# Performance work log

Hardware: AMD Instinct MI355X
Metric: run time of the kernel (lower is better)

The kernel has to match this reference:

```python
import jax, jax.numpy as jnp
import numpy as np

B, L, E, H = 4, 2048, 512, 8


def setup_inputs() -> dict:
    key = jax.random.key(0)
    ks = jax.random.split(key, 12)
    s = 0.02
    inp = {
        "values": jax.random.normal(ks[0], (B, L, E), jnp.float32),
        "keys": jax.random.normal(ks[1], (B, L, E), jnp.float32),
        "queries": jax.random.normal(ks[2], (B, L, E), jnp.float32),
    }
    mask = jax.random.randint(ks[3], (B, L, H, H), 0, 2, jnp.int32)
    # guarantee at least one unmasked entry per softmax row to avoid NaN rows
    mask = mask.at[..., 0].set(1)
    inp["mask"] = mask
    # Linear(E, E*H) weights stored as (in, out); torch uses y = x @ W.T + b
    inp["Wv"] = jax.random.normal(ks[4], (E, E * H), jnp.float32) * s
    inp["bv"] = jnp.zeros((E * H,), jnp.float32)
    inp["Wk"] = jax.random.normal(ks[5], (E, E * H), jnp.float32) * s
    inp["bk"] = jnp.zeros((E * H,), jnp.float32)
    inp["Wq"] = jax.random.normal(ks[6], (E, E * H), jnp.float32) * s
    inp["bq"] = jnp.zeros((E * H,), jnp.float32)
    inp["Wo"] = jax.random.normal(ks[7], (E * H, E), jnp.float32) * s
    inp["bo"] = jnp.zeros((E,), jnp.float32)
    return inp


def reference(values, keys, queries, mask, Wv, bv, Wk, bk, Wq, bq, Wo, bo):
    b, l, e = queries.shape
    h = Wq.shape[1] // e

    def proj(x, W, bias):
        # (B,L,E) -> (B,L,H,E) -> transpose(1,2) -> (B,H,L,E)
        return (x @ W + bias).reshape(b, -1, h, e).transpose(0, 2, 1, 3)

    v = proj(values, Wv, bv)
    k = proj(keys, Wk, bk)
    q = proj(queries, Wq, bq)
    # Faithful to source: einsum labels applied to the TRANSPOSED (B,H,L,E)
    # tensors, so 'q'/'k' bind to the heads axis and 'h' binds to seq axis.
    # energy: (B, L, H, H) -- head-vs-head scores at each position.
    energy = jnp.einsum('nqhd,nkhd->nhqk', q, k)
    energy = jnp.where(mask == 0, -jnp.inf, energy)
    attn = jax.nn.softmax(energy / jnp.sqrt(jnp.float32(e)), axis=3)
    # out of einsum: (B, H, L, E); raw row-major reshape to (B, L, H*E)
    out = jnp.einsum('nhql,nlhd->nqhd', attn, v).reshape(b, -1, h * e)
    return out @ Wo + bo
```

## Files before the change

### kernel.cpp

```cpp
#include <hip/hip_runtime.h>
#include <stdint.h>

typedef __attribute__((ext_vector_type(4))) float f32x4;
typedef __attribute__((ext_vector_type(8))) __bf16 bf16x8;

__device__ __forceinline__ unsigned short f2bf(float f) {
  union { float f; uint32_t u; } v; v.f = f;
  uint32_t u = v.u;
  return (unsigned short)((u + 0x7FFFu + ((u >> 16) & 1u)) >> 16);
}
__device__ __forceinline__ float bflo(uint32_t u) {
  union { uint32_t u; float f; } v; v.u = u << 16; return v.f;
}
__device__ __forceinline__ float bfhi(uint32_t u) {
  union { uint32_t u; float f; } v; v.u = u & 0xffff0000u; return v.f;
}

__device__ __forceinline__ void async_copy16(void* lds, const void* g) {
  __builtin_amdgcn_global_load_lds(
      (const __attribute__((address_space(1))) void*)g,
      (__attribute__((address_space(3))) void*)lds,
      16, 0, 0);
}

__global__ void cvt3_f32_bf16(const float* __restrict__ in0,
                              const float* __restrict__ in1,
                              const float* __restrict__ in2,
                              uint32_t* __restrict__ out, int n) {
  const float* in = (blockIdx.y == 0) ? in0 : (blockIdx.y == 1) ? in1 : in2;
  uint32_t* o = out + (size_t)blockIdx.y * (n / 2);
  int i = blockIdx.x * blockDim.x + threadIdx.x;
  int idx = i * 8;
  if (idx >= n) return;
  float4 a = *(const float4*)(in + idx);
  float4 b = *(const float4*)(in + idx + 4);
  uint4 ov;
  ov.x = f2bf(a.x) | ((uint32_t)f2bf(a.y) << 16);
  ov.y = f2bf(a.z) | ((uint32_t)f2bf(a.w) << 16);
  ov.z = f2bf(b.x) | ((uint32_t)f2bf(b.y) << 16);
  ov.w = f2bf(b.z) | ((uint32_t)f2bf(b.w) << 16);
  *(uint4*)(o + i * 4) = ov;
}

__global__ void transpose3_to_bf16(const float* __restrict__ in0,
                                   const float* __restrict__ in1,
                                   const float* __restrict__ in2,
                                   unsigned short* __restrict__ out,
                                   int R, int C) {
  const float* in = (blockIdx.z == 0) ? in0 : (blockIdx.z == 1) ? in1 : in2;
  unsigned short* o = out + (size_t)blockIdx.z * ((size_t)R * C);
  __shared__ float tile[32][33];
  int c0 = blockIdx.x * 32, r0 = blockIdx.y * 32;
  int tx = threadIdx.x, ty = threadIdx.y;
  #pragma unroll
  for (int rr = 0; rr < 32; rr += 8)
    tile[ty + rr][tx] = in[(size_t)(r0 + ty + rr) * C + c0 + tx];
  __syncthreads();
  #pragma unroll
  for (int rr = 0; rr < 32; rr += 8)
    o[(size_t)(c0 + ty + rr) * R + r0 + tx] = f2bf(tile[tx][ty + rr]);
}

__global__ void transpose_to_bf16(const float* __restrict__ in,
                                  unsigned short* __restrict__ out,
                                  int R, int C) {
  __shared__ float tile[32][33];
  int c0 = blockIdx.x * 32, r0 = blockIdx.y * 32;
  int tx = threadIdx.x, ty = threadIdx.y;
  #pragma unroll
  for (int rr = 0; rr < 32; rr += 8)
    tile[ty + rr][tx] = in[(size_t)(r0 + ty + rr) * C + c0 + tx];
  __syncthreads();
  #pragma unroll
  for (int rr = 0; rr < 32; rr += 8)
    out[(size_t)(c0 + ty + rr) * R + r0 + tx] = f2bf(tile[tx][ty + rr]);
}

template <int NK, int NN, bool PARTIAL>
__global__ __launch_bounds__(512, 2) void gemm256(
    const unsigned short* __restrict__ A,
    const unsigned short* __restrict__ Bt,
    const float* __restrict__ bias,
    void* __restrict__ Cout,
    int Mt, int NtG, int KC, int Kfull) {
  constexpr int TT = NK * NN;
  static_assert(TT >= 3, "schedule needs >=3 tiles");
  __shared__ unsigned short lds[2 * 2 * 256 * 64];

  const int nwg = Mt * NtG * KC;
  const int cpx = nwg >> 3;
  const int bid = blockIdx.x;
  const int nb = (bid & 7) * cpx + (bid >> 3);
  const int kc = nb / (Mt * NtG);
  const int r2 = nb % (Mt * NtG);
  const int bm = r2 / NtG;
  const int ng = r2 % NtG;
  const int N = NtG * NN * 256;
  const size_t koff = (size_t)kc * (NK * 64);

  const int tid = threadIdx.x;
  const int wv = tid >> 6, ln = tid & 63;
  const int wm = wv >> 2, wn = wv & 3;

  f32x4 acc[8][4] = {};
  bf16x8 af[4][2];
  bf16x8 bfb[2][2];

  auto stage_A = [&](int h, int tau) {
    const int kt = tau % NK;
    #pragma unroll
    for (int r = 0; r < 2; ++r) {
      const int rb = r * 128 + h * 64 + wv * 8;
      const int row = rb + (ln >> 3);
      const int kcs = (ln & 7) ^ (row & 7);
      const unsigned short* g =
          A + (size_t)(bm * 256 + row) * Kfull + koff + kt * 64 + kcs * 8;
      char* dst = (char*)lds + (size_t)(tau & 1) * 65536 + rb * 128;
      async_copy16(dst, g);
    }
  };
  auto stage_B = [&](int h, int tau) {
    const int kt = tau % NK;
    const int bnn = ng * NN + tau / NK;
    #pragma unroll
    for (int r = 0; r < 2; ++r) {
      const int s = r * 2 + (wv >> 2);
      const int rb = s * 64 + h * 32 + (wv & 3) * 8;
      const int row = rb + (ln >> 3);
      const int kcs = (ln & 7) ^ (row & 7);
      const unsigned short* g =
          Bt + (size_t)(bnn * 256 + row) * Kfull + koff + kt * 64 + kcs * 8;
      char* dst = (char*)lds + (size_t)(tau & 1) * 65536 + 32768 + rb * 128;
      async_copy16(dst, g);
    }
  };
  auto load_af = [&](int mh, const char* buf) {
    #pragma unroll
    for (int f = 0; f < 4; ++f) {
      const int lr = wm * 128 + (mh * 4 + f) * 16 + (ln & 15);
      #pragma unroll
      for (int s = 0; s < 2; ++s) {
        const int kq = s * 4 + (ln >> 4);
        af[f][s] = *(const bf16x8*)(buf + lr * 128 + ((kq ^ (lr & 7)) * 16));
      }
    }
  };
  auto load_bf = [&](int nh, const char* buf) {
    #pragma unroll
    for (int gq = 0; gq < 2; ++gq) {
      const int lr = wn * 64 + (nh * 2 + gq) * 16 + (ln & 15);
      #pragma unroll
      for (int s = 0; s < 2; ++s) {
        const int kq = s * 4 + (ln >> 4);
        bfb[gq][s] =
            *(const bf16x8*)(buf + 32768 + lr * 128 + ((kq ^ (lr & 7)) * 16));
      }
    }
  };
  auto mfma_quad = [&](int mh, int nh) {
    __builtin_amdgcn_sched_barrier(0);
    __builtin_amdgcn_s_barrier();
    __builtin_amdgcn_sched_barrier(0);
    __builtin_amdgcn_s_setprio(1);
    #pragma unroll
    for (int f = 0; f < 4; ++f)
      #pragma unroll
      for (int gq = 0; gq < 2; ++gq)
        #pragma unroll
        for (int s = 0; s < 2; ++s)
          acc[mh * 4 + f][nh * 2 + gq] = __builtin_amdgcn_mfma_f32_16x16x32_bf16(
              bfb[gq][s], af[f][s], acc[mh * 4 + f][nh * 2 + gq], 0, 0, 0);
    __builtin_amdgcn_s_setprio(0);
    __builtin_amdgcn_sched_barrier(0);
  };
  auto epilogue = [&](int nt) {
    const int m0 = bm * 256 + wm * 128 + (ln & 15);
    const int n0 = (ng * NN + nt) * 256 + wn * 64 + ((ln >> 4) << 2);
    if (PARTIAL) {
      float* Cp = (float*)Cout + (size_t)kc * ((size_t)Mt * 256) * N;
      #pragma unroll
      for (int f = 0; f < 8; ++f) {
        const int row = m0 + f * 16;
        #pragma unroll
        for (int g = 0; g < 4; ++g)
          *(f32x4*)(Cp + (size_t)row * N + n0 + g * 16) = acc[f][g];
      }
    } else {
      unsigned short* C = (unsigned short*)Cout;
      #pragma unroll
      for (int f = 0; f < 8; ++f) {
        const int row = m0 + f * 16;
        #pragma unroll
        for (int g = 0; g < 4; ++g) {
          const int col = n0 + g * 16;
          float4 bv = *(const float4*)(bias + col);
          uint2 o;
          o.x = f2bf(acc[f][g][0] + bv.x) | ((uint32_t)f2bf(acc[f][g][1] + bv.y) << 16);
          o.y = f2bf(acc[f][g][2] + bv.z) | ((uint32_t)f2bf(acc[f][g][3] + bv.w) << 16);
          *(uint2*)(C + (size_t)row * N + col) = o;
        }
      }
    }
    #pragma unroll
    for (int f = 0; f < 8; ++f)
      #pragma unroll
      for (int g = 0; g < 4; ++g)
        acc[f][g] = (f32x4){0.f, 0.f, 0.f, 0.f};
  };

  stage_A(0, 0); stage_B(1, 0); stage_A(1, 0); stage_B(0, 0);
  stage_A(0, 1); stage_B(1, 1); stage_A(1, 1);
  asm volatile("s_waitcnt vmcnt(6)" ::: "memory");
  __builtin_amdgcn_sched_barrier(0);
  __builtin_amdgcn_s_barrier();

  for (int tau = 0; tau < TT; ++tau) {
    const char* buf = (const char*)lds + (size_t)(tau & 1) * 65536;
    load_af(0, buf); load_bf(0, buf);
    if (tau + 1 < TT) stage_B(0, tau + 1);
    mfma_quad(0, 0);
    __builtin_amdgcn_s_barrier();
    load_bf(1, buf);
    if (tau + 2 < TT) stage_A(0, tau + 2);
    mfma_quad(0, 1);
    __builtin_amdgcn_s_barrier();
    load_af(1, buf);
    if (tau + 2 < TT) stage_B(1, tau + 2);
    mfma_quad(1, 1);
    __builtin_amdgcn_s_barrier();
    load_bf(0, buf);
    if (tau + 2 < TT) stage_A(1, tau + 2);
    mfma_quad(1, 0);
    if (tau + 2 < TT) {
      asm volatile("s_waitcnt vmcnt(6)" ::: "memory");
    } else if (tau + 1 < TT) {
      asm volatile("s_waitcnt vmcnt(0)" ::: "memory");
    }
    __builtin_amdgcn_sched_barrier(0);
    __builtin_amdgcn_s_barrier();
    if ((tau + 1) % NK == 0) epilogue(tau / NK);
  }
}

__global__ void reduce4_bias(const float* __restrict__ p,
                             const float* __restrict__ bo,
                             float* __restrict__ out) {
  const size_t S = (size_t)8192 * 512;
  size_t i = ((size_t)blockIdx.x * 256 + threadIdx.x) * 4;
  float4 a = *(const float4*)(p + i);
  float4 b = *(const float4*)(p + S + i);
  float4 c = *(const float4*)(p + 2 * S + i);
  float4 d = *(const float4*)(p + 3 * S + i);
  float4 bb = *(const float4*)(bo + (int)(i & 511));
  float4 o;
  o.x = a.x + b.x + c.x + d.x + bb.x;
  o.y = a.y + b.y + c.y + d.y + bb.y;
  o.z = a.z + b.z + c.z + d.z + bb.z;
  o.w = a.w + b.w + c.w + d.w + bb.w;
  *(float4*)(out + i) = o;
}

__global__ __launch_bounds__(256) void energy_mfma(
    const unsigned short* __restrict__ Q,
    const unsigned short* __restrict__ Kb,
    const int* __restrict__ mask,
    float* __restrict__ P) {
  const int wave = threadIdx.x >> 6, ln = threadIdx.x & 63;
  const int t2 = (blockIdx.x * 4 + wave) * 2;
  const int r16 = ln & 15;
  const int g = ln >> 4;
  const size_t rowoff = (size_t)(t2 + (r16 >> 3)) * 4096 + (r16 & 7) * 512 + g * 8;
  const unsigned short* qb = Q + rowoff;
  const unsigned short* kb = Kb + rowoff;

  f32x4 acc = {};
  #pragma unroll
  for (int s = 0; s < 16; ++s) {
    bf16x8 qf = *(const bf16x8*)(qb + s * 32);
    bf16x8 kf = *(const bf16x8*)(kb + s * 32);
    acc = __builtin_amdgcn_mfma_f32_16x16x32_bf16(qf, kf, acc, 0, 0, 0);
  }

  const int ct = r16 >> 3, j = r16 & 7;
  const bool valid = ((g >> 1) == ct);
  const int tok = t2 + ct;
  float pv[4];
  #pragma unroll
  for (int r = 0; r < 4; ++r) {
    const int i = (g & 1) * 4 + r;
    float e = acc[r] * 0.044194173824159216f;
    int mk = 1;
    if (valid) mk = mask[(size_t)tok * 64 + i * 8 + j];
    if (mk == 0) e = -1e30f;
    float m = e;
    m = fmaxf(m, __shfl_xor(m, 1, 64));
    m = fmaxf(m, __shfl_xor(m, 2, 64));
    m = fmaxf(m, __shfl_xor(m, 4, 64));
    float p = __expf(e - m);
    float sum = p;
    sum += __shfl_xor(sum, 1, 64);
    sum += __shfl_xor(sum, 2, 64);
    sum += __shfl_xor(sum, 4, 64);
    pv[r] = p / sum;
  }
  if (valid) {
    #pragma unroll
    for (int r = 0; r < 4; ++r) {
      const int i = (g & 1) * 4 + r;
      P[(size_t)tok * 64 + i * 8 + j] = pv[r];
    }
  }
}

__global__ __launch_bounds__(256) void pv_kernel(
    const float* __restrict__ P,
    const unsigned short* __restrict__ Vb,
    unsigned short* __restrict__ out2) {
  const int wave = threadIdx.x >> 6, lane = threadIdx.x & 63;
  const int t = blockIdx.x * 4 + wave;
  const unsigned short* Vr = Vb + (size_t)t * 4096;
  float att = P[(size_t)t * 64 + lane];

  uint4 v4[8];
  #pragma unroll
  for (int jj = 0; jj < 8; ++jj)
    v4[jj] = *(const uint4*)(Vr + jj * 512 + lane * 8);

  const int nb = t >> 11, l = t & 2047;
  const size_t tok_base = (size_t)nb * 8388608 + (size_t)(l >> 3) * 4096 +
                          (size_t)(l & 7) * 512 + lane * 8;
  #pragma unroll
  for (int hh = 0; hh < 8; ++hh) {
    float accv[8] = {0.f, 0.f, 0.f, 0.f, 0.f, 0.f, 0.f, 0.f};
    #pragma unroll
    for (int jj = 0; jj < 8; ++jj) {
      float a = __shfl(att, hh * 8 + jj, 64);
      accv[0] += a * bflo(v4[jj].x); accv[1] += a * bfhi(v4[jj].x);
      accv[2] += a * bflo(v4[jj].y); accv[3] += a * bfhi(v4[jj].y);
      accv[4] += a * bflo(v4[jj].z); accv[5] += a * bfhi(v4[jj].z);
      accv[6] += a * bflo(v4[jj].w); accv[7] += a * bfhi(v4[jj].w);
    }
    uint4 o;
    o.x = f2bf(accv[0]) | ((uint32_t)f2bf(accv[1]) << 16);
    o.y = f2bf(accv[2]) | ((uint32_t)f2bf(accv[3]) << 16);
    o.z = f2bf(accv[4]) | ((uint32_t)f2bf(accv[5]) << 16);
    o.w = f2bf(accv[6]) | ((uint32_t)f2bf(accv[7]) << 16);
    *(uint4*)(out2 + tok_base + (size_t)hh * 1048576) = o;
  }
}

extern "C" void kernel_launch(void* const* d_in, const int* in_sizes, int n_in,
                              void* d_out, int out_size, void* d_ws, size_t ws_size,
                              hipStream_t stream) {
  const float* values  = (const float*)d_in[0];
  const float* keys    = (const float*)d_in[1];
  const float* queries = (const float*)d_in[2];
  const int*   mask    = (const int*)d_in[3];
  const float* Wv = (const float*)d_in[4];
  const float* bv = (const float*)d_in[5];
  const float* Wk = (const float*)d_in[6];
  const float* bk = (const float*)d_in[7];
  const float* Wq = (const float*)d_in[8];
  const float* bq = (const float*)d_in[9];
  const float* Wo = (const float*)d_in[10];
  const float* bo = (const float*)d_in[11];

  unsigned short* xv  = (unsigned short*)d_ws;
  unsigned short* xk  = xv + 8192 * 512;
  unsigned short* xq  = xk + 8192 * 512;
  unsigned short* Wvt = xq + 8192 * 512;
  unsigned short* Wkt = Wvt + 4096 * 512;
  unsigned short* Wqt = Wkt + 4096 * 512;
  unsigned short* Wot = Wqt + 4096 * 512;
  float*          P   = (float*)(Wot + 4096 * 512);
  unsigned short* bufA = (unsigned short*)(P + 8192 * 64);
  unsigned short* bufB = bufA + (size_t)8192 * 4096;

  const int nx = 8192 * 512;
  cvt3_f32_bf16<<<dim3(nx / 8 / 256, 3), 256, 0, stream>>>(
      values, keys, queries, (uint32_t*)xv, nx);

  transpose3_to_bf16<<<dim3(4096 / 32, 512 / 32, 3), dim3(32, 8), 0, stream>>>(
      Wv, Wk, Wq, Wvt, 512, 4096);
  transpose_to_bf16<<<dim3(512 / 32, 4096 / 32), dim3(32, 8), 0, stream>>>(
      Wo, Wot, 4096, 512);

  gemm256<8, 2, false><<<256, 512, 0, stream>>>(xq, Wqt, bq, bufA, 32, 8, 1, 512);
  gemm256<8, 2, false><<<256, 512, 0, stream>>>(xk, Wkt, bk, bufB, 32, 8, 1, 512);

  energy_mfma<<<8192 / 8, 256, 0, stream>>>(bufA, bufB, mask, P);

  gemm256<8, 2, false><<<256, 512, 0, stream>>>(xv, Wvt, bv, bufA, 32, 8, 1, 512);

  pv_kernel<<<8192 / 4, 256, 0, stream>>>(P, bufA, bufB);

  gemm256<16, 1, true><<<256, 512, 0, stream>>>(bufB, Wot, nullptr, (float*)bufA,
                                                32, 2, 4, 4096);
  reduce4_bias<<<4096, 256, 0, stream>>>((float*)bufA, bo, (float*)d_out);
}
```

Before: 271.6 us.

## Fuse Q and K projection GEMMs into one launch and add smaller-tile V GEMM

Merges the Q and K projection GEMMs into a single dual-matrix launch of 512 workgroups, each picking its source matrices from its N-group index. This doubles the number of workgroups in flight, since 256 workgroups at 2 per CU underfill the GPU. The V projection moves to a new 128x128-tile GEMM kernel with 2048 workgroups and simple double buffering, trading per-tile reuse for more parallelism. The new kernel waits on vmcnt(0) every tile, so global-load latency may be less hidden than in the deeper-pipelined 256 kernel.

```diff
diff --git a/kernel.cpp b/kernel.cpp
--- a/kernel.cpp
+++ b/kernel.cpp
@@ -76,15 +76,19 @@
     out[(size_t)(c0 + ty + rr) * R + r0 + tx] = f2bf(tile[tx][ty + rr]);
 }
 
-template <int NK, int NN, bool PARTIAL>
+template <int NK, int NN, bool PARTIAL, bool DUAL>
 __global__ __launch_bounds__(512, 2) void gemm256(
     const unsigned short* __restrict__ A,
     const unsigned short* __restrict__ Bt,
     const float* __restrict__ bias,
     void* __restrict__ Cout,
+    const unsigned short* __restrict__ A2,
+    const unsigned short* __restrict__ Bt2,
+    const float* __restrict__ bias2,
+    void* __restrict__ Cout2,
     int Mt, int NtG, int KC, int Kfull) {
   constexpr int TT = NK * NN;
-  static_assert(TT >= 3, "schedule needs >=3 tiles");
+  static_assert(TT >= 4, "schedule needs >=4 tiles");
   __shared__ unsigned short lds[2 * 2 * 256 * 64];
 
   const int nwg = Mt * NtG * KC;
@@ -95,8 +99,15 @@
   const int r2 = nb % (Mt * NtG);
   const int bm = r2 / NtG;
   const int ng = r2 % NtG;
-  const int N = NtG * NN * 256;
+  const int mat = DUAL ? (ng >> 3) : 0;
+  const int ngm = DUAL ? (ng & 7) : ng;
+  const int N = (DUAL ? (NtG >> 1) : NtG) * NN * 256;
   const size_t koff = (size_t)kc * (NK * 64);
+
+  const unsigned short* Asrc = (DUAL && mat) ? A2 : A;
+  const unsigned short* Bsrc = (DUAL && mat) ? Bt2 : Bt;
+  const float* biasd = (DUAL && mat) ? bias2 : bias;
+  void* Cd = (DUAL && mat) ? Cout2 : Cout;
 
   const int tid = threadIdx.x;
   const int wv = tid >> 6, ln = tid & 63;
@@ -114,14 +125,14 @@
       const int row = rb + (ln >> 3);
       const int kcs = (ln & 7) ^ (row & 7);
       const unsigned short* g =
-          A + (size_t)(bm * 256 + row) * Kfull + koff + kt * 64 + kcs * 8;
+          Asrc + (size_t)(bm * 256 + row) * Kfull + koff + kt * 64 + kcs * 8;
       char* dst = (char*)lds + (size_t)(tau & 1) * 65536 + rb * 128;
       async_copy16(dst, g);
     }
   };
   auto stage_B = [&](int h, int tau) {
     const int kt = tau % NK;
-    const int bnn = ng * NN + tau / NK;
+    const int bnn = ngm * NN + tau / NK;
     #pragma unroll
     for (int r = 0; r < 2; ++r) {
       const int s = r * 2 + (wv >> 2);
@@ -129,7 +140,7 @@
       const int row = rb + (ln >> 3);
       const int kcs = (ln & 7) ^ (row & 7);
       const unsigned short* g =
-          Bt + (size_t)(bnn * 256 + row) * Kfull + koff + kt * 64 + kcs * 8;
+          Bsrc + (size_t)(bnn * 256 + row) * Kfull + koff + kt * 64 + kcs * 8;
       char* dst = (char*)lds + (size_t)(tau & 1) * 65536 + 32768 + rb * 128;
       async_copy16(dst, g);
     }
@@ -175,9 +186,9 @@
   };
   auto epilogue = [&](int nt) {
     const int m0 = bm * 256 + wm * 128 + (ln & 15);
-    const int n0 = (ng * NN + nt) * 256 + wn * 64 + ((ln >> 4) << 2);
+    const int n0 = (ngm * NN + nt) * 256 + wn * 64 + ((ln >> 4) << 2);
     if (PARTIAL) {
-      float* Cp = (float*)Cout + (size_t)kc * ((size_t)Mt * 256) * N;
+      float* Cp = (float*)Cd + (size_t)kc * ((size_t)Mt * 256) * N;
       #pragma unroll
       for (int f = 0; f < 8; ++f) {
         const int row = m0 + f * 16;
@@ -186,14 +197,14 @@
           *(f32x4*)(Cp + (size_t)row * N + n0 + g * 16) = acc[f][g];
       }
     } else {
-      unsigned short* C = (unsigned short*)Cout;
+      unsigned short* C = (unsigned short*)Cd;
       #pragma unroll
       for (int f = 0; f < 8; ++f) {
         const int row = m0 + f * 16;
         #pragma unroll
         for (int g = 0; g < 4; ++g) {
           const int col = n0 + g * 16;
-          float4 bv = *(const float4*)(bias + col);
+          float4 bv = *(const float4*)(biasd + col);
           uint2 o;
           o.x = f2bf(acc[f][g][0] + bv.x) | ((uint32_t)f2bf(acc[f][g][1] + bv.y) << 16);
           o.y = f2bf(acc[f][g][2] + bv.z) | ((uint32_t)f2bf(acc[f][g][3] + bv.w) << 16);
@@ -242,6 +253,106 @@
   }
 }
 
+template <int NK>
+__global__ __launch_bounds__(256, 2) void gemm128(
+    const unsigned short* __restrict__ A,
+    const unsigned short* __restrict__ Bt,
+    const float* __restrict__ bias,
+    unsigned short* __restrict__ Cout,
+    int Mt, int Nt, int Kfull) {
+  static_assert((NK % 2) == 0, "even NK");
+  __shared__ unsigned short lds[2 * 2 * 128 * 64];
+  const int nwg = Mt * Nt;
+  const int cpx = nwg >> 3;
+  const int bid = blockIdx.x;
+  const int nb = (bid & 7) * cpx + (bid >> 3);
+  const int bm = nb / Nt, bn = nb % Nt;
+  const int N = Nt * 128;
+  const int tid = threadIdx.x;
+  const int wv = tid >> 6, ln = tid & 63;
+  const int wm = wv >> 1, wn = wv & 1;
+
+  f32x4 acc[4][4] = {};
+  bf16x8 af[4][2], bfb[4][2];
+  char* const lds0 = (char*)lds;
+  char* const lds1 = (char*)lds + 32768;
+
+  auto stage = [&](int t, char* dst) {
+    #pragma unroll
+    for (int r = 0; r < 4; ++r) {
+      const int c = wv * 4 + r;
+      const int row = c * 8 + (ln >> 3);
+      const int kcs = (ln & 7) ^ (row & 7);
+      const unsigned short* ga =
+          A + (size_t)(bm * 128 + row) * Kfull + t * 64 + kcs * 8;
+      async_copy16(dst + c * 1024, ga);
+      const unsigned short* gb =
+          Bt + (size_t)(bn * 128 + row) * Kfull + t * 64 + kcs * 8;
+      async_copy16(dst + 16384 + c * 1024, gb);
+    }
+  };
+  auto tile_body = [&](int t, const char* buf, char* obuf) {
+    if (t + 1 < NK) stage(t + 1, obuf);
+    #pragma unroll
+    for (int f = 0; f < 4; ++f) {
+      const int lr = wm * 64 + f * 16 + (ln & 15);
+      #pragma unroll
+      for (int s = 0; s < 2; ++s) {
+        const int kq = s * 4 + (ln >> 4);
+        af[f][s] = *(const bf16x8*)(buf + lr * 128 + ((kq ^ (lr & 7)) * 16));
+      }
+    }
+    #pragma unroll
+    for (int c = 0; c < 4; ++c) {
+      const int lr = wn * 64 + c * 16 + (ln & 15);
+      #pragma unroll
+      for (int s = 0; s < 2; ++s) {
+        const int kq = s * 4 + (ln >> 4);
+        bfb[c][s] = *(const bf16x8*)(buf + 16384 + lr * 128 + ((kq ^ (lr & 7)) * 16));
+      }
+    }
+    __builtin_amdgcn_s_setprio(1);
+    #pragma unroll
+    for (int f = 0; f < 4; ++f)
+      #pragma unroll
+      for (int c = 0; c < 4; ++c)
+        #pragma unroll
+        for (int s = 0; s < 2; ++s)
+          acc[f][c] = __builtin_amdgcn_mfma_f32_16x16x32_bf16(
+              bfb[c][s], af[f][s], acc[f][c], 0, 0, 0);
+    __builtin_amdgcn_s_setprio(0);
+    asm volatile("s_waitcnt vmcnt(0)" ::: "memory");
+    __builtin_amdgcn_sched_barrier(0);
+    __builtin_amdgcn_s_barrier();
+  };
+
+  stage(0, lds0);
+  asm volatile("s_waitcnt vmcnt(0)" ::: "memory");
+  __builtin_amdgcn_sched_barrier(0);
+  __builtin_amdgcn_s_barrier();
+
+  for (int it = 0; it < NK / 2; ++it) {
+    tile_body(2 * it,     lds0, lds1);
+    tile_body(2 * it + 1, lds1, lds0);
+  }
+
+  const int m0 = bm * 128 + wm * 64 + (ln & 15);
+  const int n0 = bn * 128 + wn * 64 + ((ln >> 4) << 2);
+  #pragma unroll
+  for (int f = 0; f < 4; ++f) {
+    const int row = m0 + f * 16;
+    #pragma unroll
+    for (int c = 0; c < 4; ++c) {
+      const int col = n0 + c * 16;
+      float4 bv = *(const float4*)(bias + col);
+      uint2 o;
+      o.x = f2bf(acc[f][c][0] + bv.x) | ((uint32_t)f2bf(acc[f][c][1] + bv.y) << 16);
+      o.y = f2bf(acc[f][c][2] + bv.z) | ((uint32_t)f2bf(acc[f][c][3] + bv.w) << 16);
+      *(uint2*)(Cout + (size_t)row * N + col) = o;
+    }
+  }
+}
+
 __global__ void reduce4_bias(const float* __restrict__ p,
                              const float* __restrict__ bo,
                              float* __restrict__ out) {
@@ -385,16 +496,17 @@
   transpose_to_bf16<<<dim3(512 / 32, 4096 / 32), dim3(32, 8), 0, stream>>>(
       Wo, Wot, 4096, 512);
 
-  gemm256<8, 2, false><<<256, 512, 0, stream>>>(xq, Wqt, bq, bufA, 32, 8, 1, 512);
-  gemm256<8, 2, false><<<256, 512, 0, stream>>>(xk, Wkt, bk, bufB, 32, 8, 1, 512);
+  gemm256<8, 2, false, true><<<512, 512, 0, stream>>>(
+      xq, Wqt, bq, bufA, xk, Wkt, bk, bufB, 32, 16, 1, 512);
 
   energy_mfma<<<8192 / 8, 256, 0, stream>>>(bufA, bufB, mask, P);
 
-  gemm256<8, 2, false><<<256, 512, 0, stream>>>(xv, Wvt, bv, bufA, 32, 8, 1, 512);
+  gemm128<8><<<2048, 256, 0, stream>>>(xv, Wvt, bv, bufA, 64, 32, 512);
 
   pv_kernel<<<8192 / 4, 256, 0, stream>>>(P, bufA, bufB);
 
-  gemm256<16, 1, true><<<256, 512, 0, stream>>>(bufB, Wot, nullptr, (float*)bufA,
-                                                32, 2, 4, 4096);
+  gemm256<16, 1, true, false><<<256, 512, 0, stream>>>(
+      bufB, Wot, nullptr, (float*)bufA, nullptr, nullptr, nullptr, nullptr,
+      32, 2, 4, 4096);
   reduce4_bias<<<4096, 256, 0, stream>>>((float*)bufA, bo, (float*)d_out);
 }
```

Measured after the change: 274.0 us. Within noise of the previous version (+0.9%).
